# Performance work log

Hardware: AMD Instinct MI355X
Metric: run time of the kernel (lower is better)

## Reference

```python
import jax, jax.numpy as jnp
import numpy as np

N_USER, N_ITEM = 100000, 50000
E, L = 640000, 200000
F0, F1, F2 = 128, 128, 64


def _mean_agg(x_src, src, dst, n_dst):
    # gather messages from source nodes, mean-aggregate onto destination nodes
    msg = x_src[src]                                            # [E, F]
    s = jax.ops.segment_sum(msg, dst, num_segments=n_dst)       # [n_dst, F]
    cnt = jax.ops.segment_sum(jnp.ones((src.shape[0], 1), x_src.dtype), dst,
                              num_segments=n_dst)               # [n_dst, 1]
    return s / jnp.maximum(cnt, 1.0)


def _sage(x_src, x_dst, src, dst, n_dst, Wl, b, Wr):
    # PyG SAGEConv: lin_l(mean_aggr(x_src)) + lin_r(x_dst)
    agg = _mean_agg(x_src, src, dst, n_dst)
    return agg @ Wl + b + x_dst @ Wr


def setup_inputs() -> dict:
    key = jax.random.key(0)
    ks = jax.random.split(key, 20)
    inp = {}
    inp['x_user'] = jax.random.normal(ks[0], (N_USER, F0), jnp.float32)
    inp['x_item'] = jax.random.normal(ks[1], (N_ITEM, F0), jnp.float32)
    inp['src_u'] = jax.random.randint(ks[2], (E,), 0, N_USER)
    inp['dst_i'] = jax.random.randint(ks[3], (E,), 0, N_ITEM)
    inp['el_src'] = jax.random.randint(ks[4], (L,), 0, N_USER)
    inp['el_dst'] = jax.random.randint(ks[5], (L,), 0, N_ITEM)
    # SAGEConv params per edge type per layer: Wl (neighbor), bias, Wr (root)
    def w(k, fi, fo):
        return jax.random.normal(k, (fi, fo), jnp.float32) * (1.0 / np.sqrt(fi))
    inp['Wl_ui1'] = w(ks[6], F0, F1);  inp['b_ui1'] = jnp.zeros((F1,), jnp.float32)
    inp['Wr_ui1'] = w(ks[7], F0, F1)
    inp['Wl_iu1'] = w(ks[8], F0, F1);  inp['b_iu1'] = jnp.zeros((F1,), jnp.float32)
    inp['Wr_iu1'] = w(ks[9], F0, F1)
    inp['Wl_ui2'] = w(ks[10], F1, F2); inp['b_ui2'] = jnp.zeros((F2,), jnp.float32)
    inp['Wr_ui2'] = w(ks[11], F1, F2)
    inp['Wl_iu2'] = w(ks[12], F1, F2); inp['b_iu2'] = jnp.zeros((F2,), jnp.float32)
    inp['Wr_iu2'] = w(ks[13], F1, F2)
    return inp


def reference(x_user, x_item, src_u, dst_i, el_src, el_dst,
              Wl_ui1, b_ui1, Wr_ui1, Wl_iu1, b_iu1, Wr_iu1,
              Wl_ui2, b_ui2, Wr_ui2, Wl_iu2, b_iu2, Wr_iu2):
    # layer 1 (to_hetero: one SAGEConv per edge type; relu per node type; eval -> no dropout)
    h_i1 = jax.nn.relu(_sage(x_user, x_item, src_u, dst_i, N_ITEM, Wl_ui1, b_ui1, Wr_ui1))
    h_u1 = jax.nn.relu(_sage(x_item, x_user, dst_i, src_u, N_USER, Wl_iu1, b_iu1, Wr_iu1))
    # layer 2
    h_i2 = _sage(h_u1, h_i1, src_u, dst_i, N_ITEM, Wl_ui2, b_ui2, Wr_ui2)
    h_u2 = _sage(h_i1, h_u1, dst_i, src_u, N_USER, Wl_iu2, b_iu2, Wr_iu2)
    # LPsimple_classif: gather endpoints, elementwise product, sum over features
    pred = (h_u2[el_src] * h_i2[el_dst]).sum(axis=-1)           # [L]
    return pred
```

## Files before the change

### kernel.cpp

```cpp
#include <hip/hip_runtime.h>

#define NUSER 100000
#define NITEM 50000
#define NEDGE 640000
#define NLINK 200000
#define GI 49
#define GU 98
#define NB1U 782
#define NB1I 391
#define NB1G (2 * (NB1U + NB1I))
#define NBU 391
#define NBI 196
#define NBG2 (2 * (NBU + NBI))
#define FCHUNK 4096
#define FNCH 157
#define FPASS 4

typedef unsigned int  uint;
typedef unsigned short ushort_t;
typedef __attribute__((ext_vector_type(8))) short bf16x8;
typedef __attribute__((ext_vector_type(4))) float f32x4;
typedef __attribute__((ext_vector_type(4))) uint  u32x4;

__device__ __forceinline__ ushort_t f2bf(float f) {
    uint u = __float_as_uint(f);
    u += 0x7FFFu + ((u >> 16) & 1u);
    return (ushort_t)(u >> 16);
}
__device__ __forceinline__ float bf2f(ushort_t h) { return __uint_as_float(((uint)h) << 16); }
__device__ __forceinline__ float lo16f(uint u) { return __uint_as_float(u << 16); }
__device__ __forceinline__ float hi16f(uint u) { return __uint_as_float(u & 0xFFFF0000u); }

__global__ __launch_bounds__(256) void countw_kernel(
    const int* __restrict__ src, const int* __restrict__ dst,
    int* __restrict__ cnt_u, int* __restrict__ cnt_i,
    const float* __restrict__ Wl0, const float* __restrict__ Wr0,
    const float* __restrict__ Wl1, const float* __restrict__ Wr1,
    const float* __restrict__ Wl2, const float* __restrict__ Wr2,
    const float* __restrict__ Wl3, const float* __restrict__ Wr3,
    ushort_t* __restrict__ Bh0, ushort_t* __restrict__ Bl0,
    ushort_t* __restrict__ Bh1, ushort_t* __restrict__ Bl1,
    ushort_t* __restrict__ Bh2, ushort_t* __restrict__ Bl2,
    ushort_t* __restrict__ Bh3, ushort_t* __restrict__ Bl3)
{
    if (blockIdx.x < 2500) {
        int e = blockIdx.x * 256 + threadIdx.x;
        if (e >= NEDGE) return;
        atomicAdd(&cnt_u[src[e]], 1);
        atomicAdd(&cnt_i[dst[e]], 1);
        return;
    }
    int b = blockIdx.x - 2500;
    const float *Wl, *Wr; ushort_t *Bh, *Bl; int FO, t;
    if (b < 16)      { Wl = Wl0; Wr = Wr0; Bh = Bh0; Bl = Bl0; FO = 128; t = b * 256 + threadIdx.x; }
    else if (b < 32) { Wl = Wl1; Wr = Wr1; Bh = Bh1; Bl = Bl1; FO = 128; t = (b - 16) * 256 + threadIdx.x; }
    else if (b < 40) { Wl = Wl2; Wr = Wr2; Bh = Bh2; Bl = Bl2; FO = 64;  t = (b - 32) * 256 + threadIdx.x; }
    else             { Wl = Wl3; Wr = Wr3; Bh = Bh3; Bl = Bl3; FO = 64;  t = (b - 40) * 256 + threadIdx.x; }
    int lane = t & 63, ks = (t >> 6) & 3, nt = t >> 8;
    int col = nt * 16 + (lane & 15);
    int k0 = ks * 32 + (lane >> 4) * 8;
    const float* W = (col < FO) ? Wl : Wr;
    int cc = (col < FO) ? col : col - FO;
#pragma unroll
    for (int j = 0; j < 8; ++j) {
        float v = W[(size_t)(k0 + j) * FO + cc];
        ushort_t h = f2bf(v);
        Bh[(size_t)t * 8 + j] = h;
        Bl[(size_t)t * 8 + j] = f2bf(v - bf2f(h));
    }
}

__global__ __launch_bounds__(256) void scan1_kernel(
    const int* __restrict__ cnt_i, const int* __restrict__ cnt_u,
    int* __restrict__ head_i, int* __restrict__ head_u,
    int* __restrict__ bsum_i, int* __restrict__ bsum_u)
{
    __shared__ int sh[256];
    int b = blockIdx.x, t = threadIdx.x;
    const int* cnt; int* head; int* bsum; int n, cb;
    if (b < GI) { cnt = cnt_i; head = head_i; bsum = bsum_i; n = NITEM; cb = b; }
    else        { cnt = cnt_u; head = head_u; bsum = bsum_u; n = NUSER; cb = b - GI; }
    int base = cb * 1024 + t * 4;
    int4 v = {0, 0, 0, 0};
    if (base + 3 < n) v = *(const int4*)(cnt + base);
    else {
        if (base + 0 < n) v.x = cnt[base + 0];
        if (base + 1 < n) v.y = cnt[base + 1];
        if (base + 2 < n) v.z = cnt[base + 2];
    }
    int s = v.x + v.y + v.z + v.w;
    sh[t] = s;
    __syncthreads();
    for (int o = 1; o < 256; o <<= 1) {
        int a = (t >= o) ? sh[t - o] : 0;
        __syncthreads();
        sh[t] += a;
        __syncthreads();
    }
    int excl = sh[t] - s;
    if (t == 255) bsum[cb] = sh[255];
    if (base + 0 < n) head[base + 0] = excl;
    if (base + 1 < n) head[base + 1] = excl + v.x;
    if (base + 2 < n) head[base + 2] = excl + v.x + v.y;
    if (base + 3 < n) head[base + 3] = excl + v.x + v.y + v.z;
}

__global__ __launch_bounds__(256) void scan23_kernel(
    int* __restrict__ head_i, int* __restrict__ head_u,
    const int* __restrict__ bsum_i, const int* __restrict__ bsum_u)
{
    __shared__ int sh[256];
    int b = blockIdx.x, t = threadIdx.x;
    int* head; const int* bsum; int n, cb;
    if (b < GI) { head = head_i; bsum = bsum_i; n = NITEM; cb = b; }
    else        { head = head_u; bsum = bsum_u; n = NUSER; cb = b - GI; }
    sh[t] = (t < cb) ? bsum[t] : 0;
    __syncthreads();
    for (int o = 128; o >= 1; o >>= 1) {
        if (t < o) sh[t] += sh[t + o];
        __syncthreads();
    }
    int add = sh[0];
    int base = cb * 1024 + t * 4;
#pragma unroll
    for (int k = 0; k < 4; ++k)
        if (base + k < n) head[base + k] += add;
}

__device__ __forceinline__ void gemm1_body(
    const float* __restrict__ A, const ushort_t* __restrict__ Bcg,
    ushort_t* __restrict__ dstp, int n, int row0, u32x4* __restrict__ bsh)
{
#pragma unroll
    for (int i = 0; i < 4; ++i)
        bsh[i * 512 + threadIdx.x] = ((const u32x4*)Bcg)[i * 512 + threadIdx.x];
    __syncthreads();

    const int lane = threadIdx.x & 63, wv = threadIdx.x >> 6;
    const int lr = lane & 15, lg = lane >> 4;
    const int r0 = row0 + wv * 16 + lr;
    const bool rv = r0 < n;
    const float* arow = A + (size_t)r0 * 128;

    f32x4 acc[8];
#pragma unroll
    for (int ct = 0; ct < 8; ++ct) { f32x4 zz = {0.f, 0.f, 0.f, 0.f}; acc[ct] = zz; }

    f32x4 fa, fb;
#define LOAD_A1(KS)                                                            \
    {                                                                          \
        fa = f32x4{0.f, 0.f, 0.f, 0.f}; fb = fa;                               \
        if (rv) {                                                              \
            const f32x4* p = (const f32x4*)(arow + (KS) * 32 + lg * 8);        \
            fa = p[0]; fb = p[1];                                              \
        }                                                                      \
    }

    LOAD_A1(0);
#pragma unroll
    for (int ks = 0; ks < 4; ++ks) {
        float e0s[4] = {fa[0], fa[2], fb[0], fb[2]};
        float e1s[4] = {fa[1], fa[3], fb[1], fb[3]};
        uint hv[4], lv[4];
#pragma unroll
        for (int j = 0; j < 4; ++j) {
            uint au = __float_as_uint(e0s[j]);
            uint bu = __float_as_uint(e1s[j]);
            uint ah_ = au & 0xFFFF0000u, bh_ = bu & 0xFFFF0000u;
            hv[j] = (au >> 16) | bh_;
            float l0 = e0s[j] - __uint_as_float(ah_);
            float l1 = e1s[j] - __uint_as_float(bh_);
            lv[j] = (__float_as_uint(l0) >> 16) | (__float_as_uint(l1) & 0xFFFF0000u);
        }
        u32x4 hq = {hv[0], hv[1], hv[2], hv[3]};
        u32x4 lq = {lv[0], lv[1], lv[2], lv[3]};
        bf16x8 ahf = __builtin_bit_cast(bf16x8, hq);
        bf16x8 alf = __builtin_bit_cast(bf16x8, lq);
        if (ks < 3) LOAD_A1(ks + 1);

#pragma unroll
        for (int ct = 0; ct < 8; ++ct) {
            bf16x8 bh = __builtin_bit_cast(bf16x8, bsh[(ct * 4 + ks) * 64 + lane]);
            acc[ct] = __builtin_amdgcn_mfma_f32_16x16x32_bf16(ahf, bh, acc[ct], 0, 0, 0);
            acc[ct] = __builtin_amdgcn_mfma_f32_16x16x32_bf16(alf, bh, acc[ct], 0, 0, 0);
        }
    }
#undef LOAD_A1

    __syncthreads();
    ushort_t* cl = (ushort_t*)bsh;
#pragma unroll
    for (int ct = 0; ct < 8; ++ct) {
        int col = ct * 16 + lr;
#pragma unroll
        for (int r = 0; r < 4; ++r)
            cl[(wv * 16 + lg * 4 + r) * 128 + col] = f2bf(acc[ct][r]);
    }
    __syncthreads();
    int row = threadIdx.x >> 2, seg = threadIdx.x & 3;
    int grow = row0 + row;
    if (grow < n) {
        const u32x4* s = (const u32x4*)(cl + row * 128) + seg * 4;
        u32x4* d = (u32x4*)(dstp + (size_t)grow * 128) + seg * 4;
        d[0] = s[0]; d[1] = s[1]; d[2] = s[2]; d[3] = s[3];
    }
}

__global__ __launch_bounds__(512) void gemmfill_kernel(
    const float* __restrict__ xu, const float* __restrict__ xi,
    const ushort_t* __restrict__ Bh0, const ushort_t* __restrict__ Bh1,
    ushort_t* __restrict__ y0, ushort_t* __restrict__ z0,
    ushort_t* __restrict__ y1, ushort_t* __restrict__ z1,
    const int* __restrict__ src, const int* __restrict__ dst,
    int* __restrict__ head_i, int* __restrict__ head_u,
    int* __restrict__ nbr_i, int* __restrict__ nbr_u)
{
    if (blockIdx.x >= NB1G) {
        int b = blockIdx.x - NB1G;
        int pass = b / (2 * FNCH);
        int rem  = b % (2 * FNCH);
        int dir  = rem / FNCH;
        int base = (rem % FNCH) * FCHUNK;
        int e_end = min(base + FCHUNK, NEDGE);
        if (dir == 0) {
            int lo = pass * (NITEM / FPASS), hi = lo + NITEM / FPASS;
            for (int e = base + threadIdx.x; e < e_end; e += 512) {
                int d = dst[e];
                if (d >= lo && d < hi) nbr_i[atomicAdd(&head_i[d], 1)] = src[e];
            }
        } else {
            int lo = pass * (NUSER / FPASS), hi = lo + NUSER / FPASS;
            for (int e = base + threadIdx.x; e < e_end; e += 512) {
                int s = src[e];
                if (s >= lo && s < hi) nbr_u[atomicAdd(&head_u[s], 1)] = dst[e];
            }
        }
        return;
    }
    __shared__ u32x4 bsh[2048];
    int bid = blockIdx.x;
    if (bid < 2 * NB1U) {
        int rowblk = bid >> 1, cg = bid & 1;
        gemm1_body(xu, Bh0 + (size_t)cg * 16384, cg ? z0 : y0, NUSER, rowblk * 128, bsh);
    } else {
        int b2 = bid - 2 * NB1U;
        int rowblk = b2 >> 1, cg = b2 & 1;
        gemm1_body(xi, Bh1 + (size_t)cg * 16384, cg ? z1 : y1, NITEM, rowblk * 128, bsh);
    }
}

__device__ __forceinline__ void gemm2_body(
    const ushort_t* __restrict__ A,
    const ushort_t* __restrict__ Bh, const ushort_t* __restrict__ Bl,
    ushort_t* __restrict__ dstp, int n, int row0,
    u32x4* __restrict__ bshH, u32x4* __restrict__ bshL)
{
#pragma unroll
    for (int i = 0; i < 2; ++i) {
        int idx = i * 512 + threadIdx.x;
        bshH[idx] = ((const u32x4*)Bh)[idx];
        bshL[idx] = ((const u32x4*)Bl)[idx];
    }
    __syncthreads();

    const int lane = threadIdx.x & 63, wv = threadIdx.x >> 6;
    const int lr = lane & 15, lg = lane >> 4;
    const int wrow0 = row0 + wv * 32;
    const int r0 = wrow0 + lr, r1 = wrow0 + 16 + lr;

    f32x4 acc[2][4];
#pragma unroll
    for (int rt = 0; rt < 2; ++rt)
#pragma unroll
        for (int ct = 0; ct < 4; ++ct) { f32x4 zz = {0.f, 0.f, 0.f, 0.f}; acc[rt][ct] = zz; }

    u32x4 qc[2];
#define LOAD_A2(KS)                                                            \
    {                                                                          \
        int kb = (KS) * 32 + lg * 8;                                           \
        int rows[2] = {r0, r1};                                                \
        _Pragma("unroll")                                                      \
        for (int rt = 0; rt < 2; ++rt) {                                       \
            qc[rt] = u32x4{0u, 0u, 0u, 0u};                                    \
            if (rows[rt] < n)                                                  \
                qc[rt] = *(const u32x4*)(A + (size_t)rows[rt] * 128 + kb);     \
        }                                                                      \
    }

    LOAD_A2(0);
#pragma unroll
    for (int ks = 0; ks < 4; ++ks) {
        bf16x8 ah[2];
#pragma unroll
        for (int rt = 0; rt < 2; ++rt) ah[rt] = __builtin_bit_cast(bf16x8, qc[rt]);
        if (ks < 3) LOAD_A2(ks + 1);

#pragma unroll
        for (int ct = 0; ct < 4; ++ct) {
            bf16x8 bh = __builtin_bit_cast(bf16x8, bshH[(ct * 4 + ks) * 64 + lane]);
            bf16x8 bl = __builtin_bit_cast(bf16x8, bshL[(ct * 4 + ks) * 64 + lane]);
#pragma unroll
            for (int rt = 0; rt < 2; ++rt) {
                acc[rt][ct] = __builtin_amdgcn_mfma_f32_16x16x32_bf16(ah[rt], bh, acc[rt][ct], 0, 0, 0);
                acc[rt][ct] = __builtin_amdgcn_mfma_f32_16x16x32_bf16(ah[rt], bl, acc[rt][ct], 0, 0, 0);
            }
        }
    }
#undef LOAD_A2

#pragma unroll
    for (int rt = 0; rt < 2; ++rt)
#pragma unroll
        for (int ct = 0; ct < 4; ++ct) {
            int cc = ct * 16 + lr;
#pragma unroll
            for (int r = 0; r < 4; ++r) {
                int orow = wrow0 + rt * 16 + lg * 4 + r;
                if (orow < n) dstp[(size_t)orow * 64 + cc] = f2bf(acc[rt][ct][r]);
            }
        }
}

__global__ __launch_bounds__(512) void gemm2_kernel(
    const ushort_t* __restrict__ A0, const ushort_t* __restrict__ A1,
    const ushort_t* __restrict__ Bh0, const ushort_t* __restrict__ Bl0,
    const ushort_t* __restrict__ Bh1, const ushort_t* __restrict__ Bl1,
    ushort_t* __restrict__ y0, ushort_t* __restrict__ z0,
    ushort_t* __restrict__ y1, ushort_t* __restrict__ z1)
{
    __shared__ u32x4 bshH[1024];
    __shared__ u32x4 bshL[1024];
    int bid = blockIdx.x;
    if (bid < 2 * NBU) {
        int rowblk = bid >> 1, cg = bid & 1;
        gemm2_body(A0, Bh0 + (size_t)cg * 8192, Bl0 + (size_t)cg * 8192,
                   cg ? z0 : y0, NUSER, rowblk * 256, bshH, bshL);
    } else {
        int b2 = bid - 2 * NBU;
        int rowblk = b2 >> 1, cg = b2 & 1;
        gemm2_body(A1, Bh1 + (size_t)cg * 8192, Bl1 + (size_t)cg * 8192,
                   cg ? z1 : y1, NITEM, rowblk * 256, bshH, bshL);
    }
}

__global__ __launch_bounds__(256) void gather1_kernel(
    const ushort_t* __restrict__ ymsg_u, const ushort_t* __restrict__ ymsg_i,
    const int* __restrict__ nbr_i, const int* __restrict__ head_i, const int* __restrict__ cnt_i,
    const int* __restrict__ nbr_u, const int* __restrict__ head_u, const int* __restrict__ cnt_u,
    const ushort_t* __restrict__ z_i, const ushort_t* __restrict__ z_u,
    const float* __restrict__ b_ui, const float* __restrict__ b_iu,
    ushort_t* __restrict__ h1_i, ushort_t* __restrict__ h1_u)
{
    int w = (blockIdx.x << 2) + (threadIdx.x >> 6);
    const ushort_t *ym, *z; const int *nbr, *head, *cnt; const float* bias;
    ushort_t* hout; int node;
    if (w < NITEM) { ym = ymsg_u; nbr = nbr_i; head = head_i; cnt = cnt_i; z = z_i; bias = b_ui; hout = h1_i; node = w; }
    else if (w < NITEM + NUSER) { ym = ymsg_i; nbr = nbr_u; head = head_u; cnt = cnt_u; z = z_u; bias = b_iu; hout = h1_u; node = w - NITEM; }
    else return;
    int lane = threadIdx.x & 63;
    int c = cnt[node], end = head[node];
    int j = end - c;
    const uint* Y = (const uint*)ym;
    float ax = 0.f, ay = 0.f;
    for (; j + 7 < end; j += 8) {
        uint u0 = Y[(size_t)nbr[j + 0] * 64 + lane];
        uint u1 = Y[(size_t)nbr[j + 1] * 64 + lane];
        uint u2 = Y[(size_t)nbr[j + 2] * 64 + lane];
        uint u3 = Y[(size_t)nbr[j + 3] * 64 + lane];
        uint u4 = Y[(size_t)nbr[j + 4] * 64 + lane];
        uint u5 = Y[(size_t)nbr[j + 5] * 64 + lane];
        uint u6 = Y[(size_t)nbr[j + 6] * 64 + lane];
        uint u7 = Y[(size_t)nbr[j + 7] * 64 + lane];
        ax += lo16f(u0) + lo16f(u1) + lo16f(u2) + lo16f(u3)
            + lo16f(u4) + lo16f(u5) + lo16f(u6) + lo16f(u7);
        ay += hi16f(u0) + hi16f(u1) + hi16f(u2) + hi16f(u3)
            + hi16f(u4) + hi16f(u5) + hi16f(u6) + hi16f(u7);
    }
    for (; j + 1 < end; j += 2) {
        uint u0 = Y[(size_t)nbr[j + 0] * 64 + lane];
        uint u1 = Y[(size_t)nbr[j + 1] * 64 + lane];
        ax += lo16f(u0) + lo16f(u1);
        ay += hi16f(u0) + hi16f(u1);
    }
    if (j < end) {
        uint u0 = Y[(size_t)nbr[j] * 64 + lane];
        ax += lo16f(u0); ay += hi16f(u0);
    }
    float m = 1.f / fmaxf((float)c, 1.f);
    uint zu = ((const uint*)z)[(size_t)node * 64 + lane];
    float vx = fmaxf(ax * m + lo16f(zu) + bias[lane * 2], 0.f);
    float vy = fmaxf(ay * m + hi16f(zu) + bias[lane * 2 + 1], 0.f);
    ((uint*)hout)[(size_t)node * 64 + lane] = (uint)f2bf(vx) | ((uint)f2bf(vy) << 16);
}

__global__ __launch_bounds__(256) void gather2_kernel(
    const ushort_t* __restrict__ ymsg_u, const ushort_t* __restrict__ ymsg_i,
    const int* __restrict__ nbr_i, const int* __restrict__ head_i, const int* __restrict__ cnt_i,
    const int* __restrict__ nbr_u, const int* __restrict__ head_u, const int* __restrict__ cnt_u,
    const ushort_t* __restrict__ z_i, const ushort_t* __restrict__ z_u,
    const float* __restrict__ b_ui, const float* __restrict__ b_iu,
    ushort_t* __restrict__ h2_i, ushort_t* __restrict__ h2_u)
{
    int w = (blockIdx.x << 2) + (threadIdx.x >> 6);
    const ushort_t *ym, *z; const int *nbr, *head, *cnt; const float* bias;
    ushort_t* hout; int node;
    if (w < NITEM) { ym = ymsg_u; nbr = nbr_i; head = head_i; cnt = cnt_i; z = z_i; bias = b_ui; hout = h2_i; node = w; }
    else if (w < NITEM + NUSER) { ym = ymsg_i; nbr = nbr_u; head = head_u; cnt = cnt_u; z = z_u; bias = b_iu; hout = h2_u; node = w - NITEM; }
    else return;
    int lane = threadIdx.x & 63;
    int c = cnt[node], end = head[node];
    int j = end - c;
    float a = 0.f;
    for (; j + 7 < end; j += 8) {
        a += bf2f(ym[(size_t)nbr[j + 0] * 64 + lane]) + bf2f(ym[(size_t)nbr[j + 1] * 64 + lane])
           + bf2f(ym[(size_t)nbr[j + 2] * 64 + lane]) + bf2f(ym[(size_t)nbr[j + 3] * 64 + lane])
           + bf2f(ym[(size_t)nbr[j + 4] * 64 + lane]) + bf2f(ym[(size_t)nbr[j + 5] * 64 + lane])
           + bf2f(ym[(size_t)nbr[j + 6] * 64 + lane]) + bf2f(ym[(size_t)nbr[j + 7] * 64 + lane]);
    }
    for (; j + 1 < end; j += 2)
        a += bf2f(ym[(size_t)nbr[j] * 64 + lane]) + bf2f(ym[(size_t)nbr[j + 1] * 64 + lane]);
    if (j < end) a += bf2f(ym[(size_t)nbr[j] * 64 + lane]);
    float m = 1.f / fmaxf((float)c, 1.f);
    float v = a * m + bf2f(z[(size_t)node * 64 + lane]) + bias[lane];
    hout[(size_t)node * 64 + lane] = f2bf(v);
}

__global__ __launch_bounds__(256) void predict_kernel(
    const int* __restrict__ el_src, const int* __restrict__ el_dst,
    const ushort_t* __restrict__ hu, const ushort_t* __restrict__ hi,
    float* __restrict__ out)
{
    int l = (blockIdx.x << 2) + (threadIdx.x >> 6);
    if (l >= NLINK) return;
    int lane = threadIdx.x & 63;
    int u = el_src[l];
    int it = el_dst[l];
    float v = bf2f(hu[(size_t)u * 64 + lane]) * bf2f(hi[(size_t)it * 64 + lane]);
#pragma unroll
    for (int o = 32; o >= 1; o >>= 1) v += __shfl_down(v, o, 64);
    if (lane == 0) out[l] = v;
}

extern "C" void kernel_launch(void* const* d_in, const int* in_sizes, int n_in,
                              void* d_out, int out_size, void* d_ws, size_t ws_size,
                              hipStream_t stream) {
    const float* x_user = (const float*)d_in[0];
    const float* x_item = (const float*)d_in[1];
    const int*   src_u  = (const int*)d_in[2];
    const int*   dst_i  = (const int*)d_in[3];
    const int*   el_src = (const int*)d_in[4];
    const int*   el_dst = (const int*)d_in[5];
    const float* Wl_ui1 = (const float*)d_in[6];
    const float* b_ui1  = (const float*)d_in[7];
    const float* Wr_ui1 = (const float*)d_in[8];
    const float* Wl_iu1 = (const float*)d_in[9];
    const float* b_iu1  = (const float*)d_in[10];
    const float* Wr_iu1 = (const float*)d_in[11];
    const float* Wl_ui2 = (const float*)d_in[12];
    const float* b_ui2  = (const float*)d_in[13];
    const float* Wr_ui2 = (const float*)d_in[14];
    const float* Wl_iu2 = (const float*)d_in[15];
    const float* b_iu2  = (const float*)d_in[16];
    const float* Wr_iu2 = (const float*)d_in[17];
    float* out = (float*)d_out;

    int* iw     = (int*)d_ws;
    int* cnt_i  = iw;
    int* cnt_u  = iw + 50000;
    int* bsum_i = iw + 150000;
    int* bsum_u = iw + 150064;
    int* head_i = iw + 150192;
    int* head_u = iw + 200192;
    int* nbr_i  = iw + 300192;
    int* nbr_u  = iw + 940192;
    char* W8 = (char*)d_ws;
    size_t off = 6320768;
    ushort_t* Bh1u = (ushort_t*)(W8 + off); off += 65536;
    ushort_t* Bl1u = (ushort_t*)(W8 + off); off += 65536;
    ushort_t* Bh1i = (ushort_t*)(W8 + off); off += 65536;
    ushort_t* Bl1i = (ushort_t*)(W8 + off); off += 65536;
    ushort_t* Bh2u = (ushort_t*)(W8 + off); off += 32768;
    ushort_t* Bl2u = (ushort_t*)(W8 + off); off += 32768;
    ushort_t* Bh2i = (ushort_t*)(W8 + off); off += 32768;
    ushort_t* Bl2i = (ushort_t*)(W8 + off); off += 32768;
    ushort_t* h1_u = (ushort_t*)(W8 + off); off += (size_t)NUSER * 128 * 2;
    ushort_t* h1_i = (ushort_t*)(W8 + off); off += (size_t)NITEM * 128 * 2;
    size_t YB = off;
    ushort_t* ymsg_u = (ushort_t*)(W8 + YB);
    ushort_t* ymsg_i = (ushort_t*)(W8 + YB + 25600000);
    ushort_t* z_u    = (ushort_t*)(W8 + YB + 38400000);
    ushort_t* z_i    = (ushort_t*)(W8 + YB + 64000000);
    ushort_t* ymsg2_u = (ushort_t*)(W8 + YB);
    ushort_t* ymsg2_i = (ushort_t*)(W8 + YB + 12800000);
    ushort_t* z2_u    = (ushort_t*)(W8 + YB + 19200000);
    ushort_t* z2_i    = (ushort_t*)(W8 + YB + 32000000);
    ushort_t* h2_u    = (ushort_t*)(W8 + YB + 38400000);
    ushort_t* h2_i    = (ushort_t*)(W8 + YB + 51200000);

    hipMemsetAsync(d_ws, 0, 150000 * sizeof(int), stream);

    countw_kernel<<<2548, 256, 0, stream>>>(
        src_u, dst_i, cnt_u, cnt_i,
        Wl_ui1, Wr_iu1, Wl_iu1, Wr_ui1, Wl_ui2, Wr_iu2, Wl_iu2, Wr_ui2,
        Bh1u, Bl1u, Bh1i, Bl1i, Bh2u, Bl2u, Bh2i, Bl2i);

    scan1_kernel<<<GI + GU, 256, 0, stream>>>(cnt_i, cnt_u, head_i, head_u, bsum_i, bsum_u);
    scan23_kernel<<<GI + GU, 256, 0, stream>>>(head_i, head_u, bsum_i, bsum_u);

    gemmfill_kernel<<<NB1G + FPASS * 2 * FNCH, 512, 0, stream>>>(
        x_user, x_item, Bh1u, Bh1i,
        ymsg_u, z_u, ymsg_i, z_i,
        src_u, dst_i, head_i, head_u, nbr_i, nbr_u);

    gather1_kernel<<<(NITEM + NUSER) / 4, 256, 0, stream>>>(
        ymsg_u, ymsg_i, nbr_i, head_i, cnt_i, nbr_u, head_u, cnt_u,
        z_i, z_u, b_ui1, b_iu1, h1_i, h1_u);

    gemm2_kernel<<<NBG2, 512, 0, stream>>>(
        h1_u, h1_i, Bh2u, Bl2u, Bh2i, Bl2i,
        ymsg2_u, z2_u, ymsg2_i, z2_i);
    gather2_kernel<<<(NITEM + NUSER) / 4, 256, 0, stream>>>(
        ymsg2_u, ymsg2_i, nbr_i, head_i, cnt_i, nbr_u, head_u, cnt_u,
        z2_i, z2_u, b_ui2, b_iu2, h2_i, h2_u);

    predict_kernel<<<NLINK / 4, 256, 0, stream>>>(el_src, el_dst, h2_u, h2_i, out);
}
```

Before: 365.1 us.

## Build CSR counts and neighbor lists with per-window shared-memory atomics

Edge counting and CSR neighbor-list filling now assign each block a window of 512 destination nodes. Each block scans the full edge list and uses shared-memory atomics for its window. This removes the memset and the random global atomics on count and head arrays, and head now stays as the exclusive start offset, so the gather kernels compute the end from head plus count. The trade-off is that every one of the ~294 window blocks rereads all 640K edge keys, relying on L2/cache bandwidth instead of global atomic throughput.

```diff
diff --git a/kernel.cpp b/kernel.cpp
--- a/kernel.cpp
+++ b/kernel.cpp
@@ -12,9 +12,11 @@
 #define NBU 391
 #define NBI 196
 #define NBG2 (2 * (NBU + NBI))
-#define FCHUNK 4096
-#define FNCH 157
-#define FPASS 4
+#define WNODE 512
+#define NWI 98
+#define NWU 196
+#define NWF (NWI + NWU)
+#define NWPREP 24
 
 typedef unsigned int  uint;
 typedef unsigned short ushort_t;
@@ -31,7 +33,7 @@
 __device__ __forceinline__ float lo16f(uint u) { return __uint_as_float(u << 16); }
 __device__ __forceinline__ float hi16f(uint u) { return __uint_as_float(u & 0xFFFF0000u); }
 
-__global__ __launch_bounds__(256) void countw_kernel(
+__global__ __launch_bounds__(512) void countw_kernel(
     const int* __restrict__ src, const int* __restrict__ dst,
     int* __restrict__ cnt_u, int* __restrict__ cnt_i,
     const float* __restrict__ Wl0, const float* __restrict__ Wr0,
@@ -43,19 +45,30 @@
     ushort_t* __restrict__ Bh2, ushort_t* __restrict__ Bl2,
     ushort_t* __restrict__ Bh3, ushort_t* __restrict__ Bl3)
 {
-    if (blockIdx.x < 2500) {
-        int e = blockIdx.x * 256 + threadIdx.x;
-        if (e >= NEDGE) return;
-        atomicAdd(&cnt_u[src[e]], 1);
-        atomicAdd(&cnt_i[dst[e]], 1);
+    __shared__ int wcnt[WNODE];
+    int b = blockIdx.x;
+    if (b < NWF) {
+        const int* key; int* cnt; int n, lo;
+        if (b < NWI) { key = dst; cnt = cnt_i; n = NITEM; lo = b * WNODE; }
+        else         { key = src; cnt = cnt_u; n = NUSER; lo = (b - NWI) * WNODE; }
+        int hi = min(lo + WNODE, n);
+        wcnt[threadIdx.x] = 0;
+        __syncthreads();
+        for (int e = threadIdx.x; e < NEDGE; e += 512) {
+            int k = key[e];
+            if (k >= lo && k < hi) atomicAdd(&wcnt[k - lo], 1);
+        }
+        __syncthreads();
+        int node = lo + threadIdx.x;
+        if (node < hi) cnt[node] = wcnt[threadIdx.x];
         return;
     }
-    int b = blockIdx.x - 2500;
+    int g = (b - NWF) * 512 + threadIdx.x;
     const float *Wl, *Wr; ushort_t *Bh, *Bl; int FO, t;
-    if (b < 16)      { Wl = Wl0; Wr = Wr0; Bh = Bh0; Bl = Bl0; FO = 128; t = b * 256 + threadIdx.x; }
-    else if (b < 32) { Wl = Wl1; Wr = Wr1; Bh = Bh1; Bl = Bl1; FO = 128; t = (b - 16) * 256 + threadIdx.x; }
-    else if (b < 40) { Wl = Wl2; Wr = Wr2; Bh = Bh2; Bl = Bl2; FO = 64;  t = (b - 32) * 256 + threadIdx.x; }
-    else             { Wl = Wl3; Wr = Wr3; Bh = Bh3; Bl = Bl3; FO = 64;  t = (b - 40) * 256 + threadIdx.x; }
+    if (g < 4096)       { Wl = Wl0; Wr = Wr0; Bh = Bh0; Bl = Bl0; FO = 128; t = g; }
+    else if (g < 8192)  { Wl = Wl1; Wr = Wr1; Bh = Bh1; Bl = Bl1; FO = 128; t = g - 4096; }
+    else if (g < 10240) { Wl = Wl2; Wr = Wr2; Bh = Bh2; Bl = Bl2; FO = 64;  t = g - 8192; }
+    else                { Wl = Wl3; Wr = Wr3; Bh = Bh3; Bl = Bl3; FO = 64;  t = g - 10240; }
     int lane = t & 63, ks = (t >> 6) & 3, nt = t >> 8;
     int col = nt * 16 + (lane & 15);
     int k0 = ks * 32 + (lane >> 4) * 8;
@@ -212,32 +225,28 @@
     ushort_t* __restrict__ y0, ushort_t* __restrict__ z0,
     ushort_t* __restrict__ y1, ushort_t* __restrict__ z1,
     const int* __restrict__ src, const int* __restrict__ dst,
-    int* __restrict__ head_i, int* __restrict__ head_u,
+    const int* __restrict__ head_i, const int* __restrict__ head_u,
     int* __restrict__ nbr_i, int* __restrict__ nbr_u)
 {
+    __shared__ u32x4 bsh[2048];
     if (blockIdx.x >= NB1G) {
         int b = blockIdx.x - NB1G;
-        int pass = b / (2 * FNCH);
-        int rem  = b % (2 * FNCH);
-        int dir  = rem / FNCH;
-        int base = (rem % FNCH) * FCHUNK;
-        int e_end = min(base + FCHUNK, NEDGE);
-        if (dir == 0) {
-            int lo = pass * (NITEM / FPASS), hi = lo + NITEM / FPASS;
-            for (int e = base + threadIdx.x; e < e_end; e += 512) {
-                int d = dst[e];
-                if (d >= lo && d < hi) nbr_i[atomicAdd(&head_i[d], 1)] = src[e];
-            }
-        } else {
-            int lo = pass * (NUSER / FPASS), hi = lo + NUSER / FPASS;
-            for (int e = base + threadIdx.x; e < e_end; e += 512) {
-                int s = src[e];
-                if (s >= lo && s < hi) nbr_u[atomicAdd(&head_u[s], 1)] = dst[e];
+        int* wcnt = (int*)bsh;
+        const int *key, *val, *head; int* nbr; int n, lo;
+        if (b < NWI) { key = dst; val = src; head = head_i; nbr = nbr_i; n = NITEM; lo = b * WNODE; }
+        else         { key = src; val = dst; head = head_u; nbr = nbr_u; n = NUSER; lo = (b - NWI) * WNODE; }
+        int hi = min(lo + WNODE, n);
+        wcnt[threadIdx.x] = 0;
+        __syncthreads();
+        for (int e = threadIdx.x; e < NEDGE; e += 512) {
+            int k = key[e];
+            if (k >= lo && k < hi) {
+                int pos = head[k] + atomicAdd(&wcnt[k - lo], 1);
+                nbr[pos] = val[e];
             }
         }
         return;
     }
-    __shared__ u32x4 bsh[2048];
     int bid = blockIdx.x;
     if (bid < 2 * NB1U) {
         int rowblk = bid >> 1, cg = bid & 1;
@@ -358,8 +367,9 @@
     else if (w < NITEM + NUSER) { ym = ymsg_i; nbr = nbr_u; head = head_u; cnt = cnt_u; z = z_u; bias = b_iu; hout = h1_u; node = w - NITEM; }
     else return;
     int lane = threadIdx.x & 63;
-    int c = cnt[node], end = head[node];
-    int j = end - c;
+    int c = cnt[node];
+    int j = head[node];
+    int end = j + c;
     const uint* Y = (const uint*)ym;
     float ax = 0.f, ay = 0.f;
     for (; j + 7 < end; j += 8) {
@@ -408,8 +418,9 @@
     else if (w < NITEM + NUSER) { ym = ymsg_i; nbr = nbr_u; head = head_u; cnt = cnt_u; z = z_u; bias = b_iu; hout = h2_u; node = w - NITEM; }
     else return;
     int lane = threadIdx.x & 63;
-    int c = cnt[node], end = head[node];
-    int j = end - c;
+    int c = cnt[node];
+    int j = head[node];
+    int end = j + c;
     float a = 0.f;
     for (; j + 7 < end; j += 8) {
         a += bf2f(ym[(size_t)nbr[j + 0] * 64 + lane]) + bf2f(ym[(size_t)nbr[j + 1] * 64 + lane])
@@ -497,9 +508,8 @@
     ushort_t* h2_u    = (ushort_t*)(W8 + YB + 38400000);
     ushort_t* h2_i    = (ushort_t*)(W8 + YB + 51200000);
 
-    hipMemsetAsync(d_ws, 0, 150000 * sizeof(int), stream);
-
-    countw_kernel<<<2548, 256, 0, stream>>>(
+
+    countw_kernel<<<NWF + NWPREP, 512, 0, stream>>>(
         src_u, dst_i, cnt_u, cnt_i,
         Wl_ui1, Wr_iu1, Wl_iu1, Wr_ui1, Wl_ui2, Wr_iu2, Wl_iu2, Wr_ui2,
         Bh1u, Bl1u, Bh1i, Bl1i, Bh2u, Bl2u, Bh2i, Bl2i);
@@ -507,7 +517,7 @@
     scan1_kernel<<<GI + GU, 256, 0, stream>>>(cnt_i, cnt_u, head_i, head_u, bsum_i, bsum_u);
     scan23_kernel<<<GI + GU, 256, 0, stream>>>(head_i, head_u, bsum_i, bsum_u);
 
-    gemmfill_kernel<<<NB1G + FPASS * 2 * FNCH, 512, 0, stream>>>(
+    gemmfill_kernel<<<NB1G + NWF, 512, 0, stream>>>(
         x_user, x_item, Bh1u, Bh1i,
         ymsg_u, z_u, ymsg_i, z_i,
         src_u, dst_i, head_i, head_u, nbr_i, nbr_u);
```

New measurement: 974.7 us. +166.9%, slower.
